# Optimization experiments

Measured on AMD Instinct MI355X. Metric: run time of the kernel, lower is better.

Reference implementation:

```python
import jax, jax.numpy as jnp
import numpy as np

B, S, D = 32, 8192, 1024

def setup_inputs() -> dict:
    key = jax.random.key(0)
    k1, k2, k3 = jax.random.split(key, 3)
    query = jax.random.normal(k1, (B, D), dtype=jnp.float32)
    keys = jax.random.normal(k2, (B, S, D), dtype=jnp.float32)
    values = jax.random.normal(k3, (B, S, D), dtype=jnp.float32)
    return {"query": query, "keys": keys, "values": values}

def reference(query, keys, values):
    # scores: [B, S] = query . keys  (single query per batch element)
    scores = jnp.einsum('bd,bsd->bs', query, keys)
    weights = jax.nn.softmax(scores, axis=-1)          # [B, S]
    context = jnp.einsum('bs,bsd->bd', weights, values)  # [B, D]
    return (context, weights)
```

## Files before the change

### kernel.cpp

```cpp
#include <hip/hip_runtime.h>
#include <math.h>

#define B_ 32
#define S_ 8192
#define D_ 1024

__global__ __launch_bounds__(256) void k_scores(const float* __restrict__ q,
                                                const float* __restrict__ keys,
                                                float* __restrict__ scores) {
  const int b = blockIdx.y;
  const int s0 = blockIdx.x * 16;

  __shared__ float qs[D_];
  for (int i = threadIdx.x; i < D_; i += 256) qs[i] = q[b * D_ + i];
  __syncthreads();

  const int wave = threadIdx.x >> 6;
  const int lane = threadIdx.x & 63;
  const float4* qv4 = (const float4*)qs;

  for (int r = wave; r < 16; r += 4) {
    const int s = s0 + r;
    const float4* kp = (const float4*)(keys + ((size_t)b * S_ + (size_t)s) * D_);
    float acc = 0.f;
#pragma unroll
    for (int j = 0; j < 4; ++j) {
      float4 kv = kp[lane + 64 * j];
      float4 qv = qv4[lane + 64 * j];
      acc += kv.x * qv.x + kv.y * qv.y + kv.z * qv.z + kv.w * qv.w;
    }
#pragma unroll
    for (int off = 32; off > 0; off >>= 1) acc += __shfl_down(acc, off, 64);
    if (lane == 0) scores[(size_t)b * S_ + s] = acc;
  }
}

__global__ __launch_bounds__(256) void k_softmax(float* __restrict__ w) {
  const int b = blockIdx.x;
  float* wr = w + (size_t)b * S_;
  const int wave = threadIdx.x >> 6;
  const int lane = threadIdx.x & 63;

  float vals[32];
  float m = -INFINITY;
#pragma unroll
  for (int i = 0; i < 32; ++i) {
    vals[i] = wr[threadIdx.x + 256 * i];
    m = fmaxf(m, vals[i]);
  }
#pragma unroll
  for (int off = 32; off > 0; off >>= 1) m = fmaxf(m, __shfl_down(m, off, 64));

  __shared__ float redm[4];
  if (lane == 0) redm[wave] = m;
  __syncthreads();
  m = fmaxf(fmaxf(redm[0], redm[1]), fmaxf(redm[2], redm[3]));

  float sum = 0.f;
#pragma unroll
  for (int i = 0; i < 32; ++i) {
    vals[i] = expf(vals[i] - m);
    sum += vals[i];
  }
#pragma unroll
  for (int off = 32; off > 0; off >>= 1) sum += __shfl_down(sum, off, 64);

  __shared__ float reds[4];
  if (lane == 0) reds[wave] = sum;
  __syncthreads();
  sum = reds[0] + reds[1] + reds[2] + reds[3];
  const float inv = 1.f / sum;
#pragma unroll
  for (int i = 0; i < 32; ++i) wr[threadIdx.x + 256 * i] = vals[i] * inv;
}

__global__ __launch_bounds__(256) void k_ctx_partial(const float* __restrict__ w,
                                                     const float* __restrict__ values,
                                                     float* __restrict__ partial,
                                                     int schunk) {
  const int b = blockIdx.y;
  const int c = blockIdx.x;
  const int s0 = c * schunk;
  const int t = threadIdx.x;

  const float4* vp = (const float4*)(values + ((size_t)b * S_ + (size_t)s0) * D_);
  const float* wp = w + (size_t)b * S_ + s0;

  float4 acc = make_float4(0.f, 0.f, 0.f, 0.f);
#pragma unroll 4
  for (int s = 0; s < schunk; ++s) {
    const float wv = wp[s];
    const float4 v = vp[(size_t)s * 256 + t];
    acc.x += wv * v.x;
    acc.y += wv * v.y;
    acc.z += wv * v.z;
    acc.w += wv * v.w;
  }
  ((float4*)partial)[((size_t)b * gridDim.x + c) * 256 + t] = acc;
}

__global__ __launch_bounds__(256) void k_ctx_reduce(const float* __restrict__ partial,
                                                    float* __restrict__ ctx,
                                                    int nchunks) {
  const int idx = blockIdx.x * 256 + threadIdx.x;
  const int b = idx >> 10;
  const int d = idx & (D_ - 1);
  float acc = 0.f;
  for (int c = 0; c < nchunks; ++c)
    acc += partial[(((size_t)b * nchunks + c) << 10) + d];
  ctx[idx] = acc;
}

extern "C" void kernel_launch(void* const* d_in, const int* in_sizes, int n_in,
                              void* d_out, int out_size, void* d_ws, size_t ws_size,
                              hipStream_t stream) {
  const float* q      = (const float*)d_in[0];
  const float* keys   = (const float*)d_in[1];
  const float* values = (const float*)d_in[2];

  float* out     = (float*)d_out;
  float* ctx     = out;
  float* weights = out + B_ * D_;

  int nchunks = 64;
  while (nchunks > 1 && (size_t)B_ * nchunks * D_ * sizeof(float) > ws_size)
    nchunks >>= 1;
  const int schunk = S_ / nchunks;
  float* partial = (float*)d_ws;

  k_scores<<<dim3(S_ / 16, B_), 256, 0, stream>>>(q, keys, weights);
  k_softmax<<<B_, 256, 0, stream>>>(weights);
  k_ctx_partial<<<dim3(nchunks, B_), 256, 0, stream>>>(weights, values, partial, schunk);
  k_ctx_reduce<<<(B_ * D_) / 256, 256, 0, stream>>>(partial, ctx, nchunks);
}
```

Measured before the change: 399.0 us.

## Fuse softmax into score and context kernels via online partial statistics

Each score block now computes a local max and sum-of-exponentials for its 16 rows, a tiny combine kernel merges these into per-row max and inverse sum, and the context kernel normalises weights on the fly and writes them out. This removes the standalone softmax pass over the weights and its low-parallelism 32-block launch. Query is also held in registers instead of shared memory. The cost is an extra small kernel and a workspace layout that requires at least 8 chunks.

```diff
diff --git a/kernel.cpp b/kernel.cpp
--- a/kernel.cpp
+++ b/kernel.cpp
@@ -4,78 +4,79 @@
 #define B_ 32
 #define S_ 8192
 #define D_ 1024
+#define ROWS_PER_BLK 16
+#define NSCORE_BLKS (S_ / ROWS_PER_BLK)
 
 __global__ __launch_bounds__(256) void k_scores(const float* __restrict__ q,
                                                 const float* __restrict__ keys,
-                                                float* __restrict__ scores) {
+                                                float* __restrict__ scores,
+                                                float2* __restrict__ stats) {
   const int b = blockIdx.y;
-  const int s0 = blockIdx.x * 16;
-
-  __shared__ float qs[D_];
-  for (int i = threadIdx.x; i < D_; i += 256) qs[i] = q[b * D_ + i];
-  __syncthreads();
-
+  const int s0 = blockIdx.x * ROWS_PER_BLK;
   const int wave = threadIdx.x >> 6;
   const int lane = threadIdx.x & 63;
-  const float4* qv4 = (const float4*)qs;
 
-  for (int r = wave; r < 16; r += 4) {
+  const float4* q4 = (const float4*)(q + (size_t)b * D_);
+  float4 qr[4];
+#pragma unroll
+  for (int j = 0; j < 4; ++j) qr[j] = q4[lane + 64 * j];
+
+  __shared__ float sc16[ROWS_PER_BLK];
+
+  for (int r = wave; r < ROWS_PER_BLK; r += 4) {
     const int s = s0 + r;
     const float4* kp = (const float4*)(keys + ((size_t)b * S_ + (size_t)s) * D_);
     float acc = 0.f;
 #pragma unroll
     for (int j = 0; j < 4; ++j) {
-      float4 kv = kp[lane + 64 * j];
-      float4 qv = qv4[lane + 64 * j];
-      acc += kv.x * qv.x + kv.y * qv.y + kv.z * qv.z + kv.w * qv.w;
+      const float4 kv = kp[lane + 64 * j];
+      acc += kv.x * qr[j].x + kv.y * qr[j].y + kv.z * qr[j].z + kv.w * qr[j].w;
     }
 #pragma unroll
     for (int off = 32; off > 0; off >>= 1) acc += __shfl_down(acc, off, 64);
-    if (lane == 0) scores[(size_t)b * S_ + s] = acc;
+    if (lane == 0) {
+      scores[(size_t)b * S_ + s] = acc;
+      sc16[r] = acc;
+    }
+  }
+  __syncthreads();
+
+  if (threadIdx.x < 64) {
+    const float v = (lane < ROWS_PER_BLK) ? sc16[lane] : -INFINITY;
+    float m = v;
+#pragma unroll
+    for (int off = 8; off > 0; off >>= 1) m = fmaxf(m, __shfl_xor(m, off, 16));
+    float p = (lane < ROWS_PER_BLK) ? expf(v - m) : 0.f;
+#pragma unroll
+    for (int off = 8; off > 0; off >>= 1) p += __shfl_xor(p, off, 16);
+    if (lane == 0) stats[(size_t)b * NSCORE_BLKS + blockIdx.x] = make_float2(m, p);
   }
 }
 
-__global__ __launch_bounds__(256) void k_softmax(float* __restrict__ w) {
+__global__ __launch_bounds__(64) void k_combine(const float2* __restrict__ stats,
+                                                float2* __restrict__ rowstats) {
   const int b = blockIdx.x;
-  float* wr = w + (size_t)b * S_;
-  const int wave = threadIdx.x >> 6;
-  const int lane = threadIdx.x & 63;
-
-  float vals[32];
-  float m = -INFINITY;
-#pragma unroll
-  for (int i = 0; i < 32; ++i) {
-    vals[i] = wr[threadIdx.x + 256 * i];
-    m = fmaxf(m, vals[i]);
+  const int lane = threadIdx.x;
+  float m = -INFINITY, ssum = 0.f;
+  for (int c = lane; c < NSCORE_BLKS; c += 64) {
+    const float2 st = stats[(size_t)b * NSCORE_BLKS + c];
+    if (st.x > m) { ssum = ssum * expf(m - st.x) + st.y; m = st.x; }
+    else          { ssum += st.y * expf(st.x - m); }
   }
 #pragma unroll
-  for (int off = 32; off > 0; off >>= 1) m = fmaxf(m, __shfl_down(m, off, 64));
-
-  __shared__ float redm[4];
-  if (lane == 0) redm[wave] = m;
-  __syncthreads();
-  m = fmaxf(fmaxf(redm[0], redm[1]), fmaxf(redm[2], redm[3]));
-
-  float sum = 0.f;
-#pragma unroll
-  for (int i = 0; i < 32; ++i) {
-    vals[i] = expf(vals[i] - m);
-    sum += vals[i];
+  for (int off = 32; off > 0; off >>= 1) {
+    const float om = __shfl_xor(m, off, 64);
+    const float os = __shfl_xor(ssum, off, 64);
+    const float nm = fmaxf(m, om);
+    ssum = ssum * expf(m - nm) + os * expf(om - nm);
+    m = nm;
   }
-#pragma unroll
-  for (int off = 32; off > 0; off >>= 1) sum += __shfl_down(sum, off, 64);
-
-  __shared__ float reds[4];
-  if (lane == 0) reds[wave] = sum;
-  __syncthreads();
-  sum = reds[0] + reds[1] + reds[2] + reds[3];
-  const float inv = 1.f / sum;
-#pragma unroll
-  for (int i = 0; i < 32; ++i) wr[threadIdx.x + 256 * i] = vals[i] * inv;
+  if (lane == 0) rowstats[b] = make_float2(m, 1.f / ssum);
 }
 
-__global__ __launch_bounds__(256) void k_ctx_partial(const float* __restrict__ w,
+__global__ __launch_bounds__(256) void k_ctx_partial(float* __restrict__ w,
                                                      const float* __restrict__ values,
+                                                     const float2* __restrict__ rowstats,
                                                      float* __restrict__ partial,
                                                      int schunk) {
   const int b = blockIdx.y;
@@ -83,13 +84,21 @@
   const int s0 = c * schunk;
   const int t = threadIdx.x;
 
+  __shared__ float wlds[1024];
+  const float2 rs = rowstats[b];
+  for (int i = t; i < schunk; i += 256) {
+    const float sc = w[(size_t)b * S_ + s0 + i];
+    const float wi = expf(sc - rs.x) * rs.y;
+    wlds[i] = wi;
+    w[(size_t)b * S_ + s0 + i] = wi;
+  }
+  __syncthreads();
+
   const float4* vp = (const float4*)(values + ((size_t)b * S_ + (size_t)s0) * D_);
-  const float* wp = w + (size_t)b * S_ + s0;
-
   float4 acc = make_float4(0.f, 0.f, 0.f, 0.f);
 #pragma unroll 4
   for (int s = 0; s < schunk; ++s) {
-    const float wv = wp[s];
+    const float wv = wlds[s];
     const float4 v = vp[(size_t)s * 256 + t];
     acc.x += wv * v.x;
     acc.y += wv * v.y;
@@ -122,14 +131,20 @@
   float* ctx     = out;
   float* weights = out + B_ * D_;
 
+  const size_t stats_bytes    = (size_t)B_ * NSCORE_BLKS * sizeof(float2);
+  const size_t rowstats_bytes = (size_t)B_ * sizeof(float2);
   int nchunks = 64;
-  while (nchunks > 1 && (size_t)B_ * nchunks * D_ * sizeof(float) > ws_size)
+  while (nchunks > 8 &&
+         (size_t)B_ * nchunks * D_ * sizeof(float) + stats_bytes + rowstats_bytes > ws_size)
     nchunks >>= 1;
   const int schunk = S_ / nchunks;
-  float* partial = (float*)d_ws;
 
-  k_scores<<<dim3(S_ / 16, B_), 256, 0, stream>>>(q, keys, weights);
-  k_softmax<<<B_, 256, 0, stream>>>(weights);
-  k_ctx_partial<<<dim3(nchunks, B_), 256, 0, stream>>>(weights, values, partial, schunk);
+  float*  partial  = (float*)d_ws;
+  float2* stats    = (float2*)((char*)d_ws + (size_t)B_ * nchunks * D_ * sizeof(float));
+  float2* rowstats = stats + (size_t)B_ * NSCORE_BLKS;
+
+  k_scores<<<dim3(NSCORE_BLKS, B_), 256, 0, stream>>>(q, keys, weights, stats);
+  k_combine<<<B_, 64, 0, stream>>>(stats, rowstats);
+  k_ctx_partial<<<dim3(nchunks, B_), 256, 0, stream>>>(weights, values, rowstats, partial, schunk);
   k_ctx_reduce<<<(B_ * D_) / 256, 256, 0, stream>>>(partial, ctx, nchunks);
 }
```

Measured after the change: 399.0 us. About the same (-0.0%).

## Fuse scores, online softmax and context into flash-decoding kernel with finalize pass

Applied to the files above, without the earlier changes.

Replaces the four-kernel pipeline with a fused kernel that computes query-key scores per 128-row chunk and keeps a running max and sum. It accumulates the exponent-weighted values in registers, writing raw scores, partial context and per-chunk stats. A finalize kernel merges chunk stats, rescales partials into the context and normalizes the weights in place. This removes separate softmax and reduce launches and the re-read of weights. The cost is fewer blocks with serialized tile loops and barriers, which may limit memory parallelism.

```diff
diff --git a/kernel.cpp b/kernel.cpp
--- a/kernel.cpp
+++ b/kernel.cpp
@@ -4,111 +4,117 @@
 #define B_ 32
 #define S_ 8192
 #define D_ 1024
+#define NCH 64
+#define SCHUNK 128
+#define TILE 16
+#define NTILES (SCHUNK / TILE)
 
-__global__ __launch_bounds__(256) void k_scores(const float* __restrict__ q,
-                                                const float* __restrict__ keys,
-                                                float* __restrict__ scores) {
+typedef float f32x4 __attribute__((ext_vector_type(4)));
+
+__global__ __launch_bounds__(256) void k_fused(
+    const float* __restrict__ q, const float* __restrict__ keys,
+    const float* __restrict__ values, float* __restrict__ scores,
+    f32x4* __restrict__ partial, float2* __restrict__ stats) {
   const int b = blockIdx.y;
-  const int s0 = blockIdx.x * 16;
+  const int c = blockIdx.x;
+  const int s0 = c * SCHUNK;
+  const int t = threadIdx.x;
+  const int wave = t >> 6;
+  const int lane = t & 63;
 
-  __shared__ float qs[D_];
-  for (int i = threadIdx.x; i < D_; i += 256) qs[i] = q[b * D_ + i];
+  const f32x4* q4 = (const f32x4*)(q + (size_t)b * D_);
+  f32x4 qr[4];
+#pragma unroll
+  for (int j = 0; j < 4; ++j) qr[j] = q4[lane + 64 * j];
+
+  __shared__ float wtile[TILE];
+
+  f32x4 acc = {0.f, 0.f, 0.f, 0.f};
+  float m_run = -INFINITY, s_run = 0.f;
+
+  const float* kbase = keys   + ((size_t)b * S_ + s0) * D_;
+  const float* vbase = values + ((size_t)b * S_ + s0) * D_;
+  float* srow = scores + (size_t)b * S_ + s0;
+
+  for (int tl = 0; tl < NTILES; ++tl) {
+    const int r0 = tl * TILE;
+
+#pragma unroll
+    for (int rr = 0; rr < 4; ++rr) {
+      const int rl = rr * 4 + wave;
+      const f32x4* kp = (const f32x4*)(kbase + (size_t)(r0 + rl) * D_);
+      float a = 0.f;
+#pragma unroll
+      for (int j = 0; j < 4; ++j) {
+        const f32x4 kv = __builtin_nontemporal_load(kp + lane + 64 * j);
+        a += kv.x * qr[j].x + kv.y * qr[j].y + kv.z * qr[j].z + kv.w * qr[j].w;
+      }
+#pragma unroll
+      for (int off = 32; off > 0; off >>= 1) a += __shfl_down(a, off, 64);
+      if (lane == 0) {
+        wtile[rl] = a;
+        srow[r0 + rl] = a;
+      }
+    }
+    __syncthreads();
+
+    float mx = m_run;
+#pragma unroll
+    for (int i = 0; i < TILE; ++i) mx = fmaxf(mx, wtile[i]);
+    const float resc = __expf(m_run - mx);
+    acc *= resc;
+    float psum = s_run * resc;
+    const f32x4* vp = (const f32x4*)(vbase + (size_t)r0 * D_);
+#pragma unroll
+    for (int i = 0; i < TILE; ++i) {
+      const float w = __expf(wtile[i] - mx);
+      psum += w;
+      const f32x4 v = __builtin_nontemporal_load(vp + (size_t)i * 256 + t);
+      acc += w * v;
+    }
+    m_run = mx;
+    s_run = psum;
+    __syncthreads();
+  }
+
+  partial[((size_t)b * NCH + c) * 256 + t] = acc;
+  if (t == 0) stats[b * NCH + c] = make_float2(m_run, s_run);
+}
+
+__global__ __launch_bounds__(256) void k_finalize(
+    const float* __restrict__ scores,
+    const float* __restrict__ partial,
+    const float2* __restrict__ stats,
+    float* __restrict__ ctx,
+    float* __restrict__ weights) {
+  const int b = blockIdx.y;
+  const int x = blockIdx.x;
+  const int t = threadIdx.x;
+
+  const float2* st = stats + (size_t)b * NCH;
+  float m = -INFINITY;
+  for (int cc = 0; cc < NCH; ++cc) m = fmaxf(m, st[cc].x);
+  float ssum = 0.f;
+  for (int cc = 0; cc < NCH; ++cc) ssum += st[cc].y * __expf(st[cc].x - m);
+  const float inv = 1.f / ssum;
+
+  __shared__ float scl[NCH];
+  if (t < NCH) scl[t] = __expf(st[t].x - m) * inv;
   __syncthreads();
 
-  const int wave = threadIdx.x >> 6;
-  const int lane = threadIdx.x & 63;
-  const float4* qv4 = (const float4*)qs;
+  if (t < 128) {
+    const int d = x * 128 + t;
+    float a = 0.f;
+    for (int cc = 0; cc < NCH; ++cc)
+      a += partial[((size_t)b * NCH + cc) * D_ + d] * scl[cc];
+    ctx[(size_t)b * D_ + d] = a;
+  }
 
-  for (int r = wave; r < 16; r += 4) {
-    const int s = s0 + r;
-    const float4* kp = (const float4*)(keys + ((size_t)b * S_ + (size_t)s) * D_);
-    float acc = 0.f;
 #pragma unroll
-    for (int j = 0; j < 4; ++j) {
-      float4 kv = kp[lane + 64 * j];
-      float4 qv = qv4[lane + 64 * j];
-      acc += kv.x * qv.x + kv.y * qv.y + kv.z * qv.z + kv.w * qv.w;
-    }
-#pragma unroll
-    for (int off = 32; off > 0; off >>= 1) acc += __shfl_down(acc, off, 64);
-    if (lane == 0) scores[(size_t)b * S_ + s] = acc;
+  for (int i = 0; i < 4; ++i) {
+    const size_t s = (size_t)b * S_ + x * 1024 + i * 256 + t;
+    weights[s] = __expf(scores[s] - m) * inv;
   }
-}
-
-__global__ __launch_bounds__(256) void k_softmax(float* __restrict__ w) {
-  const int b = blockIdx.x;
-  float* wr = w + (size_t)b * S_;
-  const int wave = threadIdx.x >> 6;
-  const int lane = threadIdx.x & 63;
-
-  float vals[32];
-  float m = -INFINITY;
-#pragma unroll
-  for (int i = 0; i < 32; ++i) {
-    vals[i] = wr[threadIdx.x + 256 * i];
-    m = fmaxf(m, vals[i]);
-  }
-#pragma unroll
-  for (int off = 32; off > 0; off >>= 1) m = fmaxf(m, __shfl_down(m, off, 64));
-
-  __shared__ float redm[4];
-  if (lane == 0) redm[wave] = m;
-  __syncthreads();
-  m = fmaxf(fmaxf(redm[0], redm[1]), fmaxf(redm[2], redm[3]));
-
-  float sum = 0.f;
-#pragma unroll
-  for (int i = 0; i < 32; ++i) {
-    vals[i] = expf(vals[i] - m);
-    sum += vals[i];
-  }
-#pragma unroll
-  for (int off = 32; off > 0; off >>= 1) sum += __shfl_down(sum, off, 64);
-
-  __shared__ float reds[4];
-  if (lane == 0) reds[wave] = sum;
-  __syncthreads();
-  sum = reds[0] + reds[1] + reds[2] + reds[3];
-  const float inv = 1.f / sum;
-#pragma unroll
-  for (int i = 0; i < 32; ++i) wr[threadIdx.x + 256 * i] = vals[i] * inv;
-}
-
-__global__ __launch_bounds__(256) void k_ctx_partial(const float* __restrict__ w,
-                                                     const float* __restrict__ values,
-                                                     float* __restrict__ partial,
-                                                     int schunk) {
-  const int b = blockIdx.y;
-  const int c = blockIdx.x;
-  const int s0 = c * schunk;
-  const int t = threadIdx.x;
-
-  const float4* vp = (const float4*)(values + ((size_t)b * S_ + (size_t)s0) * D_);
-  const float* wp = w + (size_t)b * S_ + s0;
-
-  float4 acc = make_float4(0.f, 0.f, 0.f, 0.f);
-#pragma unroll 4
-  for (int s = 0; s < schunk; ++s) {
-    const float wv = wp[s];
-    const float4 v = vp[(size_t)s * 256 + t];
-    acc.x += wv * v.x;
-    acc.y += wv * v.y;
-    acc.z += wv * v.z;
-    acc.w += wv * v.w;
-  }
-  ((float4*)partial)[((size_t)b * gridDim.x + c) * 256 + t] = acc;
-}
-
-__global__ __launch_bounds__(256) void k_ctx_reduce(const float* __restrict__ partial,
-                                                    float* __restrict__ ctx,
-                                                    int nchunks) {
-  const int idx = blockIdx.x * 256 + threadIdx.x;
-  const int b = idx >> 10;
-  const int d = idx & (D_ - 1);
-  float acc = 0.f;
-  for (int c = 0; c < nchunks; ++c)
-    acc += partial[(((size_t)b * nchunks + c) << 10) + d];
-  ctx[idx] = acc;
 }
 
 extern "C" void kernel_launch(void* const* d_in, const int* in_sizes, int n_in,
@@ -122,14 +128,12 @@
   float* ctx     = out;
   float* weights = out + B_ * D_;
 
-  int nchunks = 64;
-  while (nchunks > 1 && (size_t)B_ * nchunks * D_ * sizeof(float) > ws_size)
-    nchunks >>= 1;
-  const int schunk = S_ / nchunks;
-  float* partial = (float*)d_ws;
+  f32x4*  partial = (f32x4*)d_ws;
+  float2* stats   = (float2*)((char*)d_ws +
+                              (size_t)B_ * NCH * D_ * sizeof(float));
 
-  k_scores<<<dim3(S_ / 16, B_), 256, 0, stream>>>(q, keys, weights);
-  k_softmax<<<B_, 256, 0, stream>>>(weights);
-  k_ctx_partial<<<dim3(nchunks, B_), 256, 0, stream>>>(weights, values, partial, schunk);
-  k_ctx_reduce<<<(B_ * D_) / 256, 256, 0, stream>>>(partial, ctx, nchunks);
+  k_fused<<<dim3(NCH, B_), 256, 0, stream>>>(q, keys, values, weights,
+                                             partial, stats);
+  k_finalize<<<dim3(8, B_), 256, 0, stream>>>(weights, (const float*)partial,
+                                              stats, ctx, weights);
 }
```

Result: faster. 345.1 us (-13.5%).
